# Kernel optimization log

Measured on AMD Instinct MI355X. Metric: run time of the kernel, lower is better.

The kernel has to match this reference:

```python
import jax, jax.numpy as jnp
import numpy as np
import math

D_MODEL = 1024
NUM_HEADS = 16
D_K = D_MODEL // NUM_HEADS
MAX_SEQ_LEN = 2048
THETA = 10000.0
BATCH = 2
SEQ = 2048


def setup_inputs() -> dict:
    key = jax.random.key(0)
    ks = jax.random.split(key, 5)
    std = math.sqrt(2.0 / (D_MODEL + D_MODEL))
    def w(k):
        return jnp.clip(std * jax.random.normal(k, (D_MODEL, D_MODEL), dtype=jnp.float32), -3 * std, 3 * std)
    return {
        "x": jax.random.normal(ks[0], (BATCH, SEQ, D_MODEL), dtype=jnp.float32),
        "token_positions": jnp.arange(SEQ, dtype=jnp.int32),
        "Wq": w(ks[1]),
        "Wk": w(ks[2]),
        "Wv": w(ks[3]),
        "Wo": w(ks[4]),
    }


def _rope_tables():
    inv_freq = 1.0 / THETA ** (jnp.arange(0, D_K, 2, dtype=jnp.float32) / D_K)  # [d_k/2]
    positions = jnp.arange(MAX_SEQ_LEN, dtype=jnp.float32)[:, None]             # [max_seq, 1]
    angles = positions * inv_freq                                               # [max_seq, d_k/2]
    return jnp.cos(angles), jnp.sin(angles)


def _apply_rope(x, cos, sin):
    # x: [..., seq, d_k]; cos/sin: [seq, d_k/2] (broadcast over leading dims)
    x1, x2 = x[..., ::2], x[..., 1::2]
    r1 = x1 * cos - x2 * sin
    r2 = x1 * sin + x2 * cos
    return jnp.stack((r1, r2), axis=-1).reshape(x.shape)


def reference(x, token_positions, Wq, Wk, Wv, Wo):
    B, S, D = x.shape
    def proj(W):
        y = jnp.einsum('bsd,od->bso', x, W)
        return y.reshape(B, S, NUM_HEADS, D_K).transpose(0, 2, 1, 3)  # [B,H,S,dk]
    q, k, v = proj(Wq), proj(Wk), proj(Wv)

    cos_t, sin_t = _rope_tables()
    cos, sin = cos_t[token_positions], sin_t[token_positions]  # [S, d_k/2]
    q = _apply_rope(q, cos, sin)
    k = _apply_rope(k, cos, sin)

    scores = jnp.einsum('bhqd,bhkd->bhqk', q, k) / math.sqrt(D_K)
    causal = jnp.tril(jnp.ones((S, S), dtype=bool))
    scores = jnp.where(causal, scores, -jnp.inf)
    attn = jax.nn.softmax(scores, axis=-1)
    out = jnp.einsum('bhqk,bhkd->bhqd', attn, v)
    out = out.transpose(0, 2, 1, 3).reshape(B, S, D)
    return jnp.einsum('bsd,od->bso', out, Wo)
```

## Files before the change

kernel.cpp:

```cpp
#include <hip/hip_runtime.h>
#include <hip/hip_bf16.h>


typedef __attribute__((ext_vector_type(8))) short short8;
typedef __attribute__((ext_vector_type(4))) float floatx4;

static __device__ __forceinline__ unsigned short f2bf(float f) {
  __hip_bfloat16 h = __float2bfloat16(f);
  return *(unsigned short*)&h;
}

static __device__ __forceinline__ unsigned int pk2bf(float a, float b) {
  unsigned int ua = __float_as_uint(a) + 0x8000u;
  unsigned int ub = __float_as_uint(b) + 0x8000u;
  return __builtin_amdgcn_perm(ub, ua, 0x07060302u);
}

static __device__ __forceinline__ float fexp2(float x) {
  float r;
  asm("v_exp_f32 %0, %1\n\ts_nop 0" : "=v"(r) : "v"(x));
  return r;
}

static __device__ __forceinline__ void gl2lds16(const unsigned short* g,
                                                unsigned short* l) {
  __builtin_amdgcn_global_load_lds(
      (const __attribute__((address_space(1))) void*)g,
      (__attribute__((address_space(3))) void*)l, 16, 0, 0);
}

__global__ __launch_bounds__(256) void cvt_all(
    const float4* __restrict__ x,  const float4* __restrict__ wq,
    const float4* __restrict__ wk, const float4* __restrict__ wv,
    const float4* __restrict__ wo,
    ushort4* __restrict__ xb,  ushort4* __restrict__ wqb,
    ushort4* __restrict__ wkb, ushort4* __restrict__ wvb,
    ushort4* __restrict__ wob,
    const int* __restrict__ tokpos,
    float* __restrict__ ctab, float* __restrict__ stab) {
  int t = blockIdx.y;
  int i = blockIdx.x * 256 + threadIdx.x;
  if (t == 5) {
    if (i < 65536) {
      int s = i >> 5, f = i & 31;
      float inv = expf(-9.210340371976184f * (float)(2 * f) / 64.0f);
      float ang = (float)tokpos[s] * inv;
      ctab[i] = cosf(ang);
      stab[i] = sinf(ang);
    }
    return;
  }
  const float4* s = (t == 0) ? x : (t == 1) ? wq : (t == 2) ? wk : (t == 3) ? wv : wo;
  ushort4* d = (t == 0) ? xb : (t == 1) ? wqb : (t == 2) ? wkb : (t == 3) ? wvb : wob;
  int n4 = (t == 0) ? 1048576 : 262144;
  if (i < n4) {
    float4 v = s[i];
    ushort4 o;
    o.x = f2bf(v.x); o.y = f2bf(v.y); o.z = f2bf(v.z); o.w = f2bf(v.w);
    d[i] = o;
  }
}

#define GEMM128_BODY(Aptr, Wptr, m0, n0)                                        \
  __shared__ __align__(16) unsigned short lA[2][128 * 64];                      \
  __shared__ __align__(16) unsigned short lB[2][128 * 64];                      \
  int tid = threadIdx.x;                                                        \
  int wave = tid >> 6, lane = tid & 63;                                         \
  int wm = wave >> 1, wn = wave & 1;                                            \
  int l15 = lane & 15, quad = lane >> 4;                                        \
  int srow = wave * 32 + (lane >> 3);                   \
  int sch = lane & 7;                                   \
  int fsw = l15 & 7;                                 \
  floatx4 acc[4][4];                                                            \
  _Pragma("unroll") for (int m = 0; m < 4; ++m)                                 \
      _Pragma("unroll") for (int n = 0; n < 4; ++n)                             \
          acc[m][n] = (floatx4){0.f, 0.f, 0.f, 0.f};                            \
  _Pragma("unroll") for (int p = 0; p < 4; ++p) {                               \
    int r = srow + p * 8;                                                       \
    int g = sch ^ (r & 7);                                                      \
    gl2lds16(Aptr + (size_t)(m0 + r) * 1024 + g * 8,                            \
             lA[0] + (wave * 32 + p * 8) * 64);                                 \
    gl2lds16(Wptr + (size_t)(n0 + r) * 1024 + g * 8,                            \
             lB[0] + (wave * 32 + p * 8) * 64);                                 \
  }                                                                             \
  __syncthreads();                                                              \
  for (int kt = 0; kt < 16; ++kt) {                                             \
    int cur = kt & 1;                                                           \
    if (kt < 15) {   \
      _Pragma("unroll") for (int p = 0; p < 4; ++p) {                           \
        int r = srow + p * 8;                                                   \
        int g = sch ^ (r & 7);                                                  \
        gl2lds16(Aptr + (size_t)(m0 + r) * 1024 + (kt + 1) * 64 + g * 8,        \
                 lA[cur ^ 1] + (wave * 32 + p * 8) * 64);                       \
        gl2lds16(Wptr + (size_t)(n0 + r) * 1024 + (kt + 1) * 64 + g * 8,        \
                 lB[cur ^ 1] + (wave * 32 + p * 8) * 64);                       \
      }                                                                         \
    }                                                                           \
    _Pragma("unroll") for (int ks = 0; ks < 2; ++ks) {                          \
      short8 af[4], bf[4];                                                      \
      _Pragma("unroll") for (int m = 0; m < 4; ++m)                             \
          af[m] = *(const short8*)(lA[cur] + (wm * 64 + m * 16 + l15) * 64 +    \
                                   (((ks * 4 + quad) ^ fsw) * 8));              \
      _Pragma("unroll") for (int n = 0; n < 4; ++n)                             \
          bf[n] = *(const short8*)(lB[cur] + (wn * 64 + n * 16 + l15) * 64 +    \
                                   (((ks * 4 + quad) ^ fsw) * 8));              \
      _Pragma("unroll") for (int m = 0; m < 4; ++m)                             \
          _Pragma("unroll") for (int n = 0; n < 4; ++n)                         \
              acc[m][n] = __builtin_amdgcn_mfma_f32_16x16x32_bf16(              \
                  af[m], bf[n], acc[m][n], 0, 0, 0);                            \
    }                                                                           \
    __syncthreads();                                                            \
  }

__global__ __launch_bounds__(256) void qkv_mfma(
    const unsigned short* __restrict__ X,
    const unsigned short* __restrict__ Wq,
    const unsigned short* __restrict__ Wk,
    const unsigned short* __restrict__ Wv,
    const float* __restrict__ ctab, const float* __restrict__ stab,
    unsigned short* __restrict__ Qo, unsigned short* __restrict__ Ko,
    unsigned short* __restrict__ Vo) {
  int mat = blockIdx.z;
  const unsigned short* W = (mat == 0) ? Wq : ((mat == 1) ? Wk : Wv);
  unsigned short* Out = (mat == 0) ? Qo : ((mat == 1) ? Ko : Vo);
  int m0 = blockIdx.x * 128, n0 = blockIdx.y * 128;

  GEMM128_BODY(X, W, m0, n0)

#pragma unroll
  for (int n = 0; n < 4; ++n) {
    int col = n0 + wn * 64 + n * 16 + l15;
    int h = col >> 6;
    int d = col & 63;
    int pi = d >> 1;
    bool odd = (d & 1) != 0;
    size_t hb = (size_t)h * 2048 * 64;
#pragma unroll
    for (int m = 0; m < 4; ++m) {
      int row0 = m0 + wm * 64 + m * 16 + quad * 4;
      int b = row0 >> 11;
      int s0 = row0 & 2047;
      size_t base = (size_t)b * 16 * 2048 * 64 + hb;
      if (mat == 2) {
        ushort4 pv;
        pv.x = f2bf(acc[m][n][0]);
        pv.y = f2bf(acc[m][n][1]);
        pv.z = f2bf(acc[m][n][2]);
        pv.w = f2bf(acc[m][n][3]);
        *(ushort4*)(Out + base + (size_t)d * 2048 + s0) = pv;
      } else {
#pragma unroll
        for (int i = 0; i < 4; ++i) {
          int s = s0 + i;
          float v = acc[m][n][i];
          float p = __shfl_xor(v, 1);
          float c = ctab[s * 32 + pi];
          float sn = stab[s * 32 + pi];
          float res = odd ? fmaf(p, sn, v * c) : fmaf(v, c, -p * sn);
          if (mat == 0) res *= 0.1803368801111204f;
          Out[base + (size_t)s * 64 + d] = f2bf(res);
        }
      }
    }
  }
}

__global__ __launch_bounds__(256) void oproj_mfma(
    const unsigned short* __restrict__ A, const unsigned short* __restrict__ Wo,
    float* __restrict__ Out) {
  __shared__ __align__(16) unsigned short lA[2][64 * 64];
  __shared__ __align__(16) unsigned short lB[2][128 * 64];
  int tid = threadIdx.x;
  int wave = tid >> 6, lane = tid & 63;
  int l15 = lane & 15, quad = lane >> 4;
  int rsub = lane >> 3, sch = lane & 7;
  int fsw = l15 & 7;
  int m0 = blockIdx.x * 64, n0 = blockIdx.y * 128;

  floatx4 acc[4][2];
#pragma unroll
  for (int m = 0; m < 4; ++m)
#pragma unroll
    for (int n = 0; n < 2; ++n) acc[m][n] = (floatx4){0.f, 0.f, 0.f, 0.f};

#pragma unroll
  for (int p = 0; p < 2; ++p) {
    int r = wave * 16 + p * 8 + rsub;
    int g = sch ^ (r & 7);
    gl2lds16(A + (size_t)(m0 + r) * 1024 + g * 8, lA[0] + (wave * 16 + p * 8) * 64);
  }
#pragma unroll
  for (int p = 0; p < 4; ++p) {
    int r = wave * 32 + p * 8 + rsub;
    int g = sch ^ (r & 7);
    gl2lds16(Wo + (size_t)(n0 + r) * 1024 + g * 8, lB[0] + (wave * 32 + p * 8) * 64);
  }
  __syncthreads();

  for (int kt = 0; kt < 16; ++kt) {
    int cur = kt & 1;
    if (kt < 15) {
#pragma unroll
      for (int p = 0; p < 2; ++p) {
        int r = wave * 16 + p * 8 + rsub;
        int g = sch ^ (r & 7);
        gl2lds16(A + (size_t)(m0 + r) * 1024 + (kt + 1) * 64 + g * 8,
                 lA[cur ^ 1] + (wave * 16 + p * 8) * 64);
      }
#pragma unroll
      for (int p = 0; p < 4; ++p) {
        int r = wave * 32 + p * 8 + rsub;
        int g = sch ^ (r & 7);
        gl2lds16(Wo + (size_t)(n0 + r) * 1024 + (kt + 1) * 64 + g * 8,
                 lB[cur ^ 1] + (wave * 32 + p * 8) * 64);
      }
    }
#pragma unroll
    for (int ks = 0; ks < 2; ++ks) {
      int slot = ((ks * 4 + quad) ^ fsw) * 8;
      short8 af[4], bf[2];
#pragma unroll
      for (int m = 0; m < 4; ++m)
        af[m] = *(const short8*)(lA[cur] + (m * 16 + l15) * 64 + slot);
#pragma unroll
      for (int n = 0; n < 2; ++n)
        bf[n] = *(const short8*)(lB[cur] + (wave * 32 + n * 16 + l15) * 64 + slot);
#pragma unroll
      for (int m = 0; m < 4; ++m)
#pragma unroll
        for (int n = 0; n < 2; ++n)
          acc[m][n] = __builtin_amdgcn_mfma_f32_16x16x32_bf16(
              af[m], bf[n], acc[m][n], 0, 0, 0);
    }
    __syncthreads();
  }

#pragma unroll
  for (int m = 0; m < 4; ++m) {
#pragma unroll
    for (int n = 0; n < 2; ++n) {
      int col = n0 + wave * 32 + n * 16 + l15;
#pragma unroll
      for (int i = 0; i < 4; ++i) {
        int row = m0 + m * 16 + quad * 4 + i;
        Out[(size_t)row * 1024 + col] = acc[m][n][i];
      }
    }
  }
}

#define LPS 72

__global__ __launch_bounds__(256) void attn_flash(
    const unsigned short* __restrict__ Q, const unsigned short* __restrict__ K,
    const unsigned short* __restrict__ Vt, unsigned short* __restrict__ Oc) {
  __shared__ __align__(16) unsigned short lK[64 * 64];
  __shared__ __align__(16) unsigned short lV[64 * 64];
  __shared__ unsigned short lP[4][16 * LPS];

  int tid = threadIdx.x;
  int wave = tid >> 6, lane = tid & 63;
  int l15 = lane & 15, quad = lane >> 4;

  int xb_ = blockIdx.x;
  int yb_ = blockIdx.y;
  int jb = yb_ >> 3, ib = yb_ & 7;
  int qtile;
  if (jb == 0)      qtile = xb_;
  else if (jb == 1) qtile = 31 - xb_;
  else if (jb == 2) qtile = (15 - xb_) & 31;
  else              qtile = (16 + xb_) & 31;
  int bh = ib * 4 + jb;

  size_t base = (size_t)bh * 2048 * 64;
  int qbase = qtile * 64;

  const unsigned short* qrow = Q + base + (size_t)(qbase + wave * 16 + l15) * 64;
  short8 qb0 = *(const short8*)(qrow + quad * 8);
  short8 qb1 = *(const short8*)(qrow + 32 + quad * 8);

  floatx4 o[4];
  float m_i = -1e30f, l_i = 0.f;
#pragma unroll
  for (int n = 0; n < 4; ++n) o[n] = (floatx4){0.f, 0.f, 0.f, 0.f};

  int r0 = tid >> 3, g = tid & 7;
  int r1 = r0 + 32;
  int e0 = g * 8;
  int sl = (g ^ (r0 & 7)) * 8;
  int fsw = l15 & 7;
  int c0 = (quad ^ fsw) * 8;
  int c1 = ((quad + 4) ^ fsw) * 8;

  const unsigned short* kp = K + base;
  const unsigned short* vp = Vt + base;
  short8 pk0 = *(const short8*)(kp + r0 * 64 + e0);
  short8 pk1 = *(const short8*)(kp + r1 * 64 + e0);
  short8 pv0 = *(const short8*)(vp + (size_t)r0 * 2048 + e0);
  short8 pv1 = *(const short8*)(vp + (size_t)r1 * 2048 + e0);

  for (int kt = 0; kt <= qtile; ++kt) {
    __syncthreads();
    *(short8*)(lK + r0 * 64 + sl) = pk0;
    *(short8*)(lK + r1 * 64 + sl) = pk1;
    *(short8*)(lV + r0 * 64 + sl) = pv0;
    *(short8*)(lV + r1 * 64 + sl) = pv1;
    __syncthreads();

    if (kt < qtile) {
      const unsigned short* kn = K + base + (size_t)(kt + 1) * 4096;
      const unsigned short* vn = Vt + base + (kt + 1) * 64;
      pk0 = *(const short8*)(kn + r0 * 64 + e0);
      pk1 = *(const short8*)(kn + r1 * 64 + e0);
      pv0 = *(const short8*)(vn + (size_t)r0 * 2048 + e0);
      pv1 = *(const short8*)(vn + (size_t)r1 * 2048 + e0);
    }

    float sc[4][4];
#pragma unroll
    for (int sub = 0; sub < 4; ++sub) {
      const unsigned short* kr = lK + (sub * 16 + l15) * 64;
      short8 a0 = *(const short8*)(kr + c0);
      short8 a1 = *(const short8*)(kr + c1);
      floatx4 s = {0.f, 0.f, 0.f, 0.f};
      s = __builtin_amdgcn_mfma_f32_16x16x32_bf16(a0, qb0, s, 0, 0, 0);
      s = __builtin_amdgcn_mfma_f32_16x16x32_bf16(a1, qb1, s, 0, 0, 0);
#pragma unroll
      for (int i = 0; i < 4; ++i) sc[sub][i] = s[i];
    }

    if (kt == qtile) {
      int qin = wave * 16 + l15;
#pragma unroll
      for (int sub = 0; sub < 4; ++sub)
#pragma unroll
        for (int i = 0; i < 4; ++i)
          if (sub * 16 + quad * 4 + i > qin) sc[sub][i] = -1e30f;
    }

    float mb = sc[0][0];
#pragma unroll
    for (int sub = 0; sub < 4; ++sub)
#pragma unroll
      for (int i = 0; i < 4; ++i) mb = fmaxf(mb, sc[sub][i]);
    mb = fmaxf(mb, __shfl_xor(mb, 16));
    mb = fmaxf(mb, __shfl_xor(mb, 32));

    float mn = fmaxf(m_i, mb);
    float al = fexp2(m_i - mn);
    m_i = mn;
    float rs = 0.f;
#pragma unroll
    for (int sub = 0; sub < 4; ++sub)
#pragma unroll
      for (int i = 0; i < 4; ++i) {
        float p = fexp2(sc[sub][i] - mn);
        sc[sub][i] = p;
        rs += p;
      }
    rs += __shfl_xor(rs, 16);
    rs += __shfl_xor(rs, 32);
    l_i = l_i * al + rs;

#pragma unroll
    for (int n = 0; n < 4; ++n) {
      o[n][0] *= al; o[n][1] *= al; o[n][2] *= al; o[n][3] *= al;
    }

    unsigned short* pw = lP[wave] + l15 * LPS;
#pragma unroll
    for (int sub = 0; sub < 4; ++sub) {
      uint2 w;
      w.x = pk2bf(sc[sub][0], sc[sub][1]);
      w.y = pk2bf(sc[sub][2], sc[sub][3]);
      *(uint2*)(pw + sub * 16 + quad * 4) = w;
    }

    const unsigned short* pr = lP[wave] + l15 * LPS + quad * 8;
    short8 pa0 = *(const short8*)(pr);
    short8 pa1 = *(const short8*)(pr + 32);

#pragma unroll
    for (int n = 0; n < 4; ++n) {
      const unsigned short* vr = lV + (n * 16 + l15) * 64;
      short8 vb0 = *(const short8*)(vr + c0);
      short8 vb1 = *(const short8*)(vr + c1);
      o[n] = __builtin_amdgcn_mfma_f32_16x16x32_bf16(vb0, pa0, o[n], 0, 0, 0);
      o[n] = __builtin_amdgcn_mfma_f32_16x16x32_bf16(vb1, pa1, o[n], 0, 0, 0);
    }
  }

  int b = bh >> 4, h = bh & 15;
  float inv = 1.f / l_i;
  int s = qbase + wave * 16 + l15;
  size_t orow = (size_t)(b * 2048 + s) * 1024 + h * 64;
#pragma unroll
  for (int n = 0; n < 4; ++n) {
    uint2 ov;
    ov.x = pk2bf(o[n][0] * inv, o[n][1] * inv);
    ov.y = pk2bf(o[n][2] * inv, o[n][3] * inv);
    *(uint2*)(Oc + orow + n * 16 + quad * 4) = ov;
  }
}

extern "C" void kernel_launch(void* const* d_in, const int* in_sizes, int n_in,
                              void* d_out, int out_size, void* d_ws, size_t ws_size,
                              hipStream_t stream) {
  const float* x  = (const float*)d_in[0];
  const int* tokpos = (const int*)d_in[1];
  const float* Wq = (const float*)d_in[2];
  const float* Wk = (const float*)d_in[3];
  const float* Wv = (const float*)d_in[4];
  const float* Wo = (const float*)d_in[5];
  float* out = (float*)d_out;

  float* ws = (float*)d_ws;
  float* ctab = ws;
  float* stab = ctab + 65536;
  unsigned short* u = (unsigned short*)(stab + 65536);
  unsigned short* Qb  = u;
  unsigned short* Kb  = Qb + 4194304;
  unsigned short* Vb  = Kb + 4194304;
  unsigned short* Oc  = Vb + 4194304;
  unsigned short* xb  = Oc + 4194304;
  unsigned short* Wqb = xb + 4194304;
  unsigned short* Wkb = Wqb + 1048576;
  unsigned short* Wvb = Wkb + 1048576;
  unsigned short* Wob = Wvb + 1048576;

  cvt_all<<<dim3(4096, 6), 256, 0, stream>>>(
      (const float4*)x, (const float4*)Wq, (const float4*)Wk,
      (const float4*)Wv, (const float4*)Wo,
      (ushort4*)xb, (ushort4*)Wqb, (ushort4*)Wkb, (ushort4*)Wvb, (ushort4*)Wob,
      tokpos, ctab, stab);

  qkv_mfma<<<dim3(32, 8, 3), 256, 0, stream>>>(
      xb, Wqb, Wkb, Wvb, ctab, stab, Qb, Kb, Vb);
  attn_flash<<<dim3(32, 32), 256, 0, stream>>>(Qb, Kb, Vb, Oc);
  oproj_mfma<<<dim3(64, 8), 256, 0, stream>>>(Oc, Wob, out);
}
```

Baseline: 195.0 us.

## Prefetch two K-tiles ahead with partial vmcnt waits in projection GEMMs

Restructures the double-buffered GEMM loops in the QKV and output projections so two K-tiles are in flight. Each iteration waits with s_waitcnt vmcnt(N) only for the older tile instead of a full __syncthreads drain. Raw s_barrier calls are placed around the buffer refill. The intent is to hide more global-to-LDS load latency behind MFMA work. The explicit vmcnt counts must match the number of issued loads per thread, or a race follows.

```diff
diff --git a/kernel.cpp b/kernel.cpp
--- a/kernel.cpp
+++ b/kernel.cpp
@@ -75,6 +75,7 @@
   _Pragma("unroll") for (int m = 0; m < 4; ++m)                                 \
       _Pragma("unroll") for (int n = 0; n < 4; ++n)                             \
           acc[m][n] = (floatx4){0.f, 0.f, 0.f, 0.f};                            \
+                    \
   _Pragma("unroll") for (int p = 0; p < 4; ++p) {                               \
     int r = srow + p * 8;                                                       \
     int g = sch ^ (r & 7);                                                      \
@@ -83,19 +84,18 @@
     gl2lds16(Wptr + (size_t)(n0 + r) * 1024 + g * 8,                            \
              lB[0] + (wave * 32 + p * 8) * 64);                                 \
   }                                                                             \
-  __syncthreads();                                                              \
+  _Pragma("unroll") for (int p = 0; p < 4; ++p) {                               \
+    int r = srow + p * 8;                                                       \
+    int g = sch ^ (r & 7);                                                      \
+    gl2lds16(Aptr + (size_t)(m0 + r) * 1024 + 64 + g * 8,                       \
+             lA[1] + (wave * 32 + p * 8) * 64);                                 \
+    gl2lds16(Wptr + (size_t)(n0 + r) * 1024 + 64 + g * 8,                       \
+             lB[1] + (wave * 32 + p * 8) * 64);                                 \
+  }                                                                             \
+  asm volatile("s_waitcnt vmcnt(8)" ::: "memory");               \
+  __builtin_amdgcn_s_barrier();                                                 \
   for (int kt = 0; kt < 16; ++kt) {                                             \
     int cur = kt & 1;                                                           \
-    if (kt < 15) {   \
-      _Pragma("unroll") for (int p = 0; p < 4; ++p) {                           \
-        int r = srow + p * 8;                                                   \
-        int g = sch ^ (r & 7);                                                  \
-        gl2lds16(Aptr + (size_t)(m0 + r) * 1024 + (kt + 1) * 64 + g * 8,        \
-                 lA[cur ^ 1] + (wave * 32 + p * 8) * 64);                       \
-        gl2lds16(Wptr + (size_t)(n0 + r) * 1024 + (kt + 1) * 64 + g * 8,        \
-                 lB[cur ^ 1] + (wave * 32 + p * 8) * 64);                       \
-      }                                                                         \
-    }                                                                           \
     _Pragma("unroll") for (int ks = 0; ks < 2; ++ks) {                          \
       short8 af[4], bf[4];                                                      \
       _Pragma("unroll") for (int m = 0; m < 4; ++m)                             \
@@ -109,7 +109,22 @@
               acc[m][n] = __builtin_amdgcn_mfma_f32_16x16x32_bf16(              \
                   af[m], bf[n], acc[m][n], 0, 0, 0);                            \
     }                                                                           \
-    __syncthreads();                                                            \
+    if (kt == 15) break;                                                        \
+    __builtin_amdgcn_s_barrier();                                      \
+    if (kt < 14) {                                                              \
+      _Pragma("unroll") for (int p = 0; p < 4; ++p) {                           \
+        int r = srow + p * 8;                                                   \
+        int g = sch ^ (r & 7);                                                  \
+        gl2lds16(Aptr + (size_t)(m0 + r) * 1024 + (kt + 2) * 64 + g * 8,        \
+                 lA[cur] + (wave * 32 + p * 8) * 64);                           \
+        gl2lds16(Wptr + (size_t)(n0 + r) * 1024 + (kt + 2) * 64 + g * 8,        \
+                 lB[cur] + (wave * 32 + p * 8) * 64);                           \
+      }                                                                         \
+      asm volatile("s_waitcnt vmcnt(8)" ::: "memory");        \
+    } else {                                                                    \
+      asm volatile("s_waitcnt vmcnt(0)" ::: "memory");         \
+    }                                                                           \
+    __builtin_amdgcn_s_barrier();                                      \
   }
 
 __global__ __launch_bounds__(256) void qkv_mfma(
@@ -184,55 +199,66 @@
     for (int n = 0; n < 2; ++n) acc[m][n] = (floatx4){0.f, 0.f, 0.f, 0.f};
 
 #pragma unroll
-  for (int p = 0; p < 2; ++p) {
-    int r = wave * 16 + p * 8 + rsub;
-    int g = sch ^ (r & 7);
-    gl2lds16(A + (size_t)(m0 + r) * 1024 + g * 8, lA[0] + (wave * 16 + p * 8) * 64);
-  }
-#pragma unroll
-  for (int p = 0; p < 4; ++p) {
-    int r = wave * 32 + p * 8 + rsub;
-    int g = sch ^ (r & 7);
-    gl2lds16(Wo + (size_t)(n0 + r) * 1024 + g * 8, lB[0] + (wave * 32 + p * 8) * 64);
-  }
-  __syncthreads();
+  for (int kp = 0; kp < 2; ++kp) {
+#pragma unroll
+    for (int p = 0; p < 2; ++p) {
+      int r = wave * 16 + p * 8 + rsub;
+      int g = sch ^ (r & 7);
+      gl2lds16(A + (size_t)(m0 + r) * 1024 + kp * 64 + g * 8,
+               lA[kp] + (wave * 16 + p * 8) * 64);
+    }
+#pragma unroll
+    for (int p = 0; p < 4; ++p) {
+      int r = wave * 32 + p * 8 + rsub;
+      int g = sch ^ (r & 7);
+      gl2lds16(Wo + (size_t)(n0 + r) * 1024 + kp * 64 + g * 8,
+               lB[kp] + (wave * 32 + p * 8) * 64);
+    }
+  }
+  asm volatile("s_waitcnt vmcnt(6)" ::: "memory");
+  __builtin_amdgcn_s_barrier();
 
   for (int kt = 0; kt < 16; ++kt) {
     int cur = kt & 1;
-    if (kt < 15) {
+#pragma unroll
+    for (int ks = 0; ks < 2; ++ks) {
+      int slot = ((ks * 4 + quad) ^ fsw) * 8;
+      short8 af[4], bf[2];
+#pragma unroll
+      for (int m = 0; m < 4; ++m)
+        af[m] = *(const short8*)(lA[cur] + (m * 16 + l15) * 64 + slot);
+#pragma unroll
+      for (int n = 0; n < 2; ++n)
+        bf[n] = *(const short8*)(lB[cur] + (wave * 32 + n * 16 + l15) * 64 + slot);
+#pragma unroll
+      for (int m = 0; m < 4; ++m)
+#pragma unroll
+        for (int n = 0; n < 2; ++n)
+          acc[m][n] = __builtin_amdgcn_mfma_f32_16x16x32_bf16(
+              af[m], bf[n], acc[m][n], 0, 0, 0);
+    }
+    if (kt == 15) break;
+    __builtin_amdgcn_s_barrier();
+    if (kt < 14) {
 #pragma unroll
       for (int p = 0; p < 2; ++p) {
         int r = wave * 16 + p * 8 + rsub;
         int g = sch ^ (r & 7);
-        gl2lds16(A + (size_t)(m0 + r) * 1024 + (kt + 1) * 64 + g * 8,
-                 lA[cur ^ 1] + (wave * 16 + p * 8) * 64);
+        gl2lds16(A + (size_t)(m0 + r) * 1024 + (kt + 2) * 64 + g * 8,
+                 lA[cur] + (wave * 16 + p * 8) * 64);
       }
 #pragma unroll
       for (int p = 0; p < 4; ++p) {
         int r = wave * 32 + p * 8 + rsub;
         int g = sch ^ (r & 7);
-        gl2lds16(Wo + (size_t)(n0 + r) * 1024 + (kt + 1) * 64 + g * 8,
-                 lB[cur ^ 1] + (wave * 32 + p * 8) * 64);
+        gl2lds16(Wo + (size_t)(n0 + r) * 1024 + (kt + 2) * 64 + g * 8,
+                 lB[cur] + (wave * 32 + p * 8) * 64);
       }
-    }
-#pragma unroll
-    for (int ks = 0; ks < 2; ++ks) {
-      int slot = ((ks * 4 + quad) ^ fsw) * 8;
-      short8 af[4], bf[2];
-#pragma unroll
-      for (int m = 0; m < 4; ++m)
-        af[m] = *(const short8*)(lA[cur] + (m * 16 + l15) * 64 + slot);
-#pragma unroll
-      for (int n = 0; n < 2; ++n)
-        bf[n] = *(const short8*)(lB[cur] + (wave * 32 + n * 16 + l15) * 64 + slot);
-#pragma unroll
-      for (int m = 0; m < 4; ++m)
-#pragma unroll
-        for (int n = 0; n < 2; ++n)
-          acc[m][n] = __builtin_amdgcn_mfma_f32_16x16x32_bf16(
-              af[m], bf[n], acc[m][n], 0, 0, 0);
-    }
-    __syncthreads();
+      asm volatile("s_waitcnt vmcnt(6)" ::: "memory");
+    } else {
+      asm volatile("s_waitcnt vmcnt(0)" ::: "memory");
+    }
+    __builtin_amdgcn_s_barrier();
   }
 
 #pragma unroll
```

Result: faster. 186.3 us (-4.4%).
